# Optimization experiments

Hardware: AMD Instinct MI355X
Metric: run time of the kernel (lower is better)

## Reference

```python
import jax, jax.numpy as jnp
import numpy as np

TOP_K = 2

def moe_linear(x, router_w, experts_w):
    # x: [T, din]; router_w: [din, E]; experts_w: [E, din, dout]
    T = x.shape[0]
    E = experts_w.shape[0]
    probs = jax.nn.softmax(x @ router_w, axis=-1)            # [T, E]
    topv, topi = jax.lax.top_k(probs, TOP_K)                 # [T, k]
    topv = topv / jnp.sum(topv, axis=-1, keepdims=True)      # renormalize over selected experts
    w = jnp.zeros((T, E), x.dtype).at[jnp.arange(T)[:, None], topi].set(topv)  # dense routing weights
    y = jnp.zeros((T, experts_w.shape[2]), x.dtype)
    for e in range(E):  # small fixed expert loop; avoids [T,E,dout] intermediate
        y = y + w[:, e:e+1] * (x @ experts_w[e])
    return y

def setup_inputs() -> dict:
    key = jax.random.key(0)
    ks = jax.random.split(key, 7)
    B, S, H, I, E = 4, 2048, 1024, 3584, 8
    sH, sI = 1.0 / np.sqrt(H), 1.0 / np.sqrt(I)
    return {
        "hidden_state": jax.random.normal(ks[0], (B, S, H), jnp.float32),
        "gate_router": jax.random.normal(ks[1], (H, E), jnp.float32) * sH,
        "gate_experts": jax.random.normal(ks[2], (E, H, I), jnp.float32) * sH,
        "up_router": jax.random.normal(ks[3], (H, E), jnp.float32) * sH,
        "up_experts": jax.random.normal(ks[4], (E, H, I), jnp.float32) * sH,
        "down_router": jax.random.normal(ks[5], (I, E), jnp.float32) * sI,
        "down_experts": jax.random.normal(ks[6], (E, I, H), jnp.float32) * sI,
    }

def reference(hidden_state, gate_router, gate_experts, up_router, up_experts, down_router, down_experts):
    B, S, H = hidden_state.shape
    x = hidden_state.reshape(B * S, H)
    g = moe_linear(x, gate_router, gate_experts)             # [T, I]
    u = moe_linear(x, up_router, up_experts)                 # [T, I]
    h = jax.nn.silu(g) * u                                   # SwiGLU
    y = moe_linear(h, down_router, down_experts)             # [T, H]
    return y.reshape(B, S, H)
```

## Files before the change

kernel.cpp:

```cpp
#include <hip/hip_runtime.h>
#include <stdint.h>
#include <stdio.h>

#define T_TOK 8192
#define HDIM  1024
#define IDIM  3584
#define NEXP  8
#define NPAIR (T_TOK*2)
#define BK 32

typedef float          f32x4 __attribute__((ext_vector_type(4)));
typedef short          s16x8 __attribute__((ext_vector_type(8)));
typedef unsigned short u16x4 __attribute__((ext_vector_type(4)));
typedef unsigned short u16x8 __attribute__((ext_vector_type(8)));

__device__ __forceinline__ unsigned short f2bf_rne(float f) {
  unsigned u = __float_as_uint(f);
  u += 0x7FFFu + ((u >> 16) & 1u);
  return (unsigned short)(u >> 16);
}
__device__ __forceinline__ float bf2f(unsigned short h) {
  return __uint_as_float(((unsigned)h) << 16);
}

__device__ __forceinline__ void gld16(const void* gsrc, void* ldst) {
  typedef const unsigned int __attribute__((address_space(1))) GU;
  typedef unsigned int       __attribute__((address_space(3))) LU;
  __builtin_amdgcn_global_load_lds((GU*)(unsigned long long)gsrc,
                                   (LU*)(unsigned int)(unsigned long long)ldst,
                                   16, 0, 0);
}

__device__ __forceinline__ void top2_write(const float* acc, int t,
                                           int* __restrict__ topi,
                                           float* __restrict__ topw) {
  int i0 = 0; float l0 = acc[0];
#pragma unroll
  for (int e = 1; e < NEXP; e++) if (acc[e] > l0) { l0 = acc[e]; i0 = e; }
  int i1 = -1; float l1 = -3.4e38f;
#pragma unroll
  for (int e = 0; e < NEXP; e++) if (e != i0 && acc[e] > l1) { l1 = acc[e]; i1 = e; }
  float w0 = 1.f/(1.f + expf(l1 - l0));
  float w1 = 1.f/(1.f + expf(l0 - l1));
  topi[2*t]   = i0; topi[2*t+1] = i1;
  topw[2*t]   = w0; topw[2*t+1] = w1;
}

__global__ __launch_bounds__(256) void split_router(
    const float* __restrict__ X,
    const float* __restrict__ RWg, const float* __restrict__ RWu,
    unsigned short* __restrict__ xhi, unsigned short* __restrict__ xlo,
    int* __restrict__ tig, float* __restrict__ twg,
    int* __restrict__ tiu, float* __restrict__ twu) {
  int lane = threadIdx.x & 63;
  int t = blockIdx.x*4 + (threadIdx.x>>6);
  const f32x4* xr = (const f32x4*)(X + (long)t*HDIM);
  u16x4* hr = (u16x4*)(xhi + (long)t*HDIM);
  u16x4* lr = (u16x4*)(xlo + (long)t*HDIM);
  float ag[NEXP], au[NEXP];
#pragma unroll
  for (int e = 0; e < NEXP; e++) { ag[e] = 0.f; au[e] = 0.f; }
#pragma unroll
  for (int it = 0; it < HDIM/4/64; it++) {
    int c4 = it*64 + lane;
    f32x4 xv = xr[c4];
    u16x4 hh, ll;
#pragma unroll
    for (int j = 0; j < 4; j++) {
      unsigned short hb = f2bf_rne(xv[j]);
      hh[j] = hb;
      ll[j] = f2bf_rne(xv[j] - bf2f(hb));
    }
    hr[c4] = hh; lr[c4] = ll;
#pragma unroll
    for (int j = 0; j < 4; j++) {
      const float* wg = RWg + (long)(c4*4+j)*NEXP;
      const float* wu = RWu + (long)(c4*4+j)*NEXP;
#pragma unroll
      for (int e = 0; e < NEXP; e++) { ag[e] += xv[j]*wg[e]; au[e] += xv[j]*wu[e]; }
    }
  }
#pragma unroll
  for (int e = 0; e < NEXP; e++) {
    float vg = ag[e], vu = au[e];
#pragma unroll
    for (int o = 1; o < 64; o <<= 1) { vg += __shfl_xor(vg, o); vu += __shfl_xor(vu, o); }
    ag[e] = vg; au[e] = vu;
  }
  if (lane == 0) { top2_write(ag, t, tig, twg); top2_write(au, t, tiu, twu); }
}

__global__ void transpose_split3(const float* __restrict__ gex,
                                 unsigned short* __restrict__ wg_hi,
                                 unsigned short* __restrict__ wg_lo,
                                 const float* __restrict__ uex,
                                 unsigned short* __restrict__ wu_hi,
                                 unsigned short* __restrict__ wu_lo,
                                 const float* __restrict__ dex,
                                 unsigned short* __restrict__ wd_hi) {
  __shared__ float t[32][33];
  int z = blockIdx.z;
  const float* W; unsigned short *hi, *lo; int K, N, k0, n0;
  if (z < NEXP)        { W = gex; hi = wg_hi; lo = wg_lo; K = HDIM; N = IDIM;
                         n0 = blockIdx.x*32; k0 = blockIdx.y*32; }
  else if (z < 2*NEXP) { W = uex; hi = wu_hi; lo = wu_lo; K = HDIM; N = IDIM;
                         n0 = blockIdx.x*32; k0 = blockIdx.y*32; }
  else                 { W = dex; hi = wd_hi; lo = nullptr; K = IDIM; N = HDIM;
                         k0 = blockIdx.x*32; n0 = blockIdx.y*32; }
  long base = (long)(z & 7) * K * N;
  int id = threadIdx.y*8 + threadIdx.x;
  int lrr = id >> 3, lcq = id & 7;
  f32x4 v = *(const f32x4*)&W[base + (long)(k0+lrr)*N + n0 + lcq*4];
  t[lrr][lcq*4+0] = v[0]; t[lrr][lcq*4+1] = v[1];
  t[lrr][lcq*4+2] = v[2]; t[lrr][lcq*4+3] = v[3];
  __syncthreads();
  int n = threadIdx.y, kq = threadIdx.x;
  u16x4 h, l;
#pragma unroll
  for (int r = 0; r < 4; r++) {
    float f = t[kq*4+r][n];
    unsigned short hb = f2bf_rne(f);
    h[r] = hb;
    l[r] = f2bf_rne(f - bf2f(hb));
  }
  long o = base + (long)(n0+n)*K + k0 + kq*4;
  *(u16x4*)&hi[o] = h;
  if (lo) *(u16x4*)&lo[o] = l;
}

__device__ __forceinline__ void perm_body(const int* __restrict__ topi,
                                          const float* __restrict__ topw,
                                          int* __restrict__ offs,
                                          int* __restrict__ ptok,
                                          float* __restrict__ pw, int e) {
  int tid = threadIdx.x, lane = tid & 63, wv = tid >> 6;
  __shared__ int cnt[NEXP];
  __shared__ int wsum[4];
  if (tid < NEXP) cnt[tid] = 0;
  __syncthreads();
  for (int p = tid; p < NPAIR; p += 256) atomicAdd(&cnt[topi[p]], 1);
  __syncthreads();
  int base = 0;
#pragma unroll
  for (int e2 = 0; e2 < NEXP; e2++) if (e2 < e) base += cnt[e2];
  if (tid == 0) { offs[e] = base; if (e == NEXP-1) offs[NEXP] = base + cnt[e]; }
  for (int p0 = 0; p0 < NPAIR; p0 += 256) {
    int p = p0 + tid;
    bool m = (topi[p] == e);
    unsigned long long b = __ballot(m);
    int lp = __popcll(b & ((1ull << lane) - 1ull));
    if (lane == 0) wsum[wv] = __popcll(b);
    __syncthreads();
    int woff = 0;
#pragma unroll
    for (int w2 = 0; w2 < 4; w2++) if (w2 < wv) woff += wsum[w2];
    int tot = wsum[0] + wsum[1] + wsum[2] + wsum[3];
    if (m) { int dst = base + woff + lp; ptok[dst] = p >> 1; pw[dst] = topw[p]; }
    base += tot;
    __syncthreads();
  }
}
__global__ __launch_bounds__(256) void build_perm(const int* topi, const float* topw,
                                                  int* offs, int* ptok, float* pw) {
  perm_body(topi, topw, offs, ptok, pw, blockIdx.x);
}
__global__ __launch_bounds__(256) void build_perm2(
    const int* tig, const float* twg, int* offsg, int* ptokg, float* pwg,
    const int* tiu, const float* twu, int* offsu, int* ptoku, float* pwu) {
  if (blockIdx.x < NEXP) perm_body(tig, twg, offsg, ptokg, pwg, blockIdx.x);
  else                   perm_body(tiu, twu, offsu, ptoku, pwu, blockIdx.x - NEXP);
}

__global__ __launch_bounds__(512) void moe_gemm3_mt(
    const unsigned short* __restrict__ Ahi, const unsigned short* __restrict__ Alo,
    const unsigned short* __restrict__ Bhi, const unsigned short* __restrict__ Blo,
    const int* __restrict__ offs, const int* __restrict__ ptok,
    const float* __restrict__ pw, float* __restrict__ out)
{
  const int e = blockIdx.z;
  const int beg = offs[e];
  const int cnt = offs[e+1] - beg;
  const int m0 = blockIdx.y * 256;
  if (m0 >= cnt) return;
  const int n0 = blockIdx.x * 256;

  __shared__ unsigned short As[2][2][256*32];
  __shared__ unsigned short Bs[2][2][256*32];
  __shared__ int   stok[256];
  __shared__ float swt[256];

  const int tid = threadIdx.x, lane = tid & 63, wv = tid >> 6;
  if (tid < 256) {
    int i = m0 + tid;
    stok[tid] = ptok[beg + (i < cnt ? i : 0)];
    swt[tid]  = (i < cnt) ? pw[beg + i] : 0.f;
  }
  __syncthreads();

  const int srow = lane >> 2;
  const int lc   = ((lane & 3) - ((lane >> 3) & 3)) & 3;
  const long aoff0 = (long)stok[wv*32 +      srow]*HDIM + lc*8;
  const long aoff1 = (long)stok[wv*32 + 16 + srow]*HDIM + lc*8;
  const long boff0 = ((long)e*IDIM + n0 + wv*32 +      srow)*HDIM + lc*8;
  const long boff1 = ((long)e*IDIM + n0 + wv*32 + 16 + srow)*HDIM + lc*8;
  const int dst0 = (wv*32     )*32;
  const int dst1 = (wv*32 + 16)*32;

#define STAGE_A(buf, kk) do {                                   \
    int kl_ = (kk)*32;                                          \
    gld16(Ahi + aoff0 + kl_, &As[buf][0][dst0]);                \
    gld16(Ahi + aoff1 + kl_, &As[buf][0][dst1]);                \
    gld16(Alo + aoff0 + kl_, &As[buf][1][dst0]);                \
    gld16(Alo + aoff1 + kl_, &As[buf][1][dst1]);                \
  } while (0)
#define STAGE_B(buf, kk) do {                                   \
    int kl_ = (kk)*32;                                          \
    gld16(Bhi + boff0 + kl_, &Bs[buf][0][dst0]);                \
    gld16(Bhi + boff1 + kl_, &Bs[buf][0][dst1]);                \
    gld16(Blo + boff0 + kl_, &Bs[buf][1][dst0]);                \
    gld16(Blo + boff1 + kl_, &Bs[buf][1][dst1]);                \
  } while (0)

  const int fl = lane & 15, fg = lane >> 4;
  const int pks = (((fg + (fl >> 1)) & 3) << 3);
  const int wm = wv >> 2, wn = wv & 3;
  const int arow = wm * 128;
  const int bcol = wn * 64;

  f32x4 acc[8][4];
#pragma unroll
  for (int m = 0; m < 8; m++)
#pragma unroll
    for (int n = 0; n < 4; n++) acc[m][n] = {0.f, 0.f, 0.f, 0.f};

  STAGE_A(0, 0);
  STAGE_B(0, 0);
  __syncthreads();

  int cur = 0;
  for (int kt = 0; kt < HDIM/BK; ++kt) {
    const bool st = (kt + 1 < HDIM/BK);
    s16x8 ahf[8], bhi4[4], blo4[4];

    if (st) STAGE_A(cur^1, kt + 1);
#pragma unroll
    for (int n = 0; n < 4; n++)
      bhi4[n] = *(const s16x8*)&Bs[cur][0][(bcol + n*16 + fl)*32 + pks];
#pragma unroll
    for (int n = 0; n < 4; n++)
      blo4[n] = *(const s16x8*)&Bs[cur][1][(bcol + n*16 + fl)*32 + pks];
#pragma unroll
    for (int i = 0; i < 8; i++)
      ahf[i] = *(const s16x8*)&As[cur][0][(arow + i*16 + fl)*32 + pks];
    __builtin_amdgcn_s_setprio(1);
#pragma unroll
    for (int i = 0; i < 8; i++)
#pragma unroll
      for (int n = 0; n < 4; n++)
        acc[i][n] = __builtin_amdgcn_mfma_f32_16x16x32_bf16(ahf[i], bhi4[n], acc[i][n], 0,0,0);
    __builtin_amdgcn_s_setprio(0);

    if (st) STAGE_B(cur^1, kt + 1);
    __builtin_amdgcn_s_setprio(1);
#pragma unroll
    for (int i = 0; i < 8; i++)
#pragma unroll
      for (int n = 0; n < 4; n++)
        acc[i][n] = __builtin_amdgcn_mfma_f32_16x16x32_bf16(ahf[i], blo4[n], acc[i][n], 0,0,0);
    __builtin_amdgcn_s_setprio(0);

#pragma unroll
    for (int i = 0; i < 8; i++)
      ahf[i] = *(const s16x8*)&As[cur][1][(arow + i*16 + fl)*32 + pks];
    __builtin_amdgcn_s_setprio(1);
#pragma unroll
    for (int i = 0; i < 8; i++)
#pragma unroll
      for (int n = 0; n < 4; n++)
        acc[i][n] = __builtin_amdgcn_mfma_f32_16x16x32_bf16(ahf[i], bhi4[n], acc[i][n], 0,0,0);
    __builtin_amdgcn_s_setprio(0);

    __syncthreads();
    cur ^= 1;
  }
#undef STAGE_A
#undef STAGE_B

#pragma unroll
  for (int m = 0; m < 8; m++)
#pragma unroll
    for (int r = 0; r < 4; r++) {
      int lrow = arow + m*16 + fg*4 + r;
      if (m0 + lrow < cnt) {
        float wt = swt[lrow];
        long ob = (long)stok[lrow]*IDIM + n0 + bcol + fl;
#pragma unroll
        for (int n = 0; n < 4; n++)
          atomicAdd(&out[ob + n*16], wt * acc[m][n][r]);
      }
    }
}

__global__ __launch_bounds__(256) void swiglu_router_bf(
    const float* __restrict__ g, const float* __restrict__ u,
    unsigned short* __restrict__ hb,
    const float* __restrict__ RW,
    int* __restrict__ topi, float* __restrict__ topw) {
  int lane = threadIdx.x & 63;
  int t = blockIdx.x*4 + (threadIdx.x>>6);
  const f32x4* gr = (const f32x4*)(g + (long)t*IDIM);
  const f32x4* ur = (const f32x4*)(u + (long)t*IDIM);
  u16x4*       hr = (u16x4*)(hb + (long)t*IDIM);
  float acc[NEXP];
#pragma unroll
  for (int e = 0; e < NEXP; e++) acc[e] = 0.f;
#pragma unroll
  for (int it = 0; it < IDIM/4/64; it++) {
    int c4 = it*64 + lane;
    f32x4 gv = gr[c4], uv = ur[c4], hv;
    u16x4 hh;
#pragma unroll
    for (int j = 0; j < 4; j++) {
      float x = gv[j];
      hv[j] = x * uv[j] / (1.f + expf(-x));
      hh[j] = f2bf_rne(hv[j]);
    }
    hr[c4] = hh;
#pragma unroll
    for (int j = 0; j < 4; j++) {
      const float* wr = RW + (long)(c4*4+j)*NEXP;
#pragma unroll
      for (int e = 0; e < NEXP; e++) acc[e] += hv[j]*wr[e];
    }
  }
#pragma unroll
  for (int e = 0; e < NEXP; e++) {
    float v = acc[e];
#pragma unroll
    for (int o = 1; o < 64; o <<= 1) v += __shfl_xor(v, o);
    acc[e] = v;
  }
  if (lane == 0) top2_write(acc, t, topi, topw);
}

__global__ __launch_bounds__(256) void moe_gemm_down_bf(
    const unsigned short* __restrict__ Hb, const unsigned short* __restrict__ Bw,
    const int* __restrict__ offs, const int* __restrict__ ptok,
    const float* __restrict__ pw, float* __restrict__ out)
{
  const int K = IDIM, N = HDIM;
  const int e = blockIdx.z;
  const int beg = offs[e];
  const int cnt = offs[e+1] - beg;
  const int m0 = blockIdx.y * 128;
  if (m0 >= cnt) return;
  const int n0 = blockIdx.x * 128;

  __shared__ unsigned short As[2][128*32], Bs[2][128*32];
  __shared__ int   stok[128];
  __shared__ float swt[128];

  const int tid = threadIdx.x, lane = tid & 63, wv = tid >> 6;
  if (tid < 128) {
    int i = m0 + tid;
    stok[tid] = ptok[beg + (i < cnt ? i : 0)];
    swt[tid]  = (i < cnt) ? pw[beg + i] : 0.f;
  }
  __syncthreads();

  const int srow = lane >> 2;
  const int lc   = ((lane & 3) - ((lane >> 3) & 3)) & 3;
  const long aoff0 = (long)stok[wv*32 +      srow]*K + lc*8;
  const long aoff1 = (long)stok[wv*32 + 16 + srow]*K + lc*8;
  const long boff0 = ((long)e*N + n0 + wv*32 +      srow)*K + lc*8;
  const long boff1 = ((long)e*N + n0 + wv*32 + 16 + srow)*K + lc*8;
  const int dst0 = (wv*32     )*32;
  const int dst1 = (wv*32 + 16)*32;

#define STAGE(buf, kt) do {                                 \
    int kl_ = (kt)*32;                                      \
    gld16(Hb + aoff0 + kl_, &As[buf][dst0]);                \
    gld16(Hb + aoff1 + kl_, &As[buf][dst1]);                \
    gld16(Bw + boff0 + kl_, &Bs[buf][dst0]);                \
    gld16(Bw + boff1 + kl_, &Bs[buf][dst1]);                \
  } while (0)

  const int fl = lane & 15, fg = lane >> 4;
  const int pks = (((fg + (fl >> 1)) & 3) << 3);
  const int arow = (wv >> 1)*64, bcol = (wv & 1)*64;

  f32x4 acc[4][4];
#pragma unroll
  for (int m = 0; m < 4; m++)
#pragma unroll
    for (int n = 0; n < 4; n++) acc[m][n] = {0.f, 0.f, 0.f, 0.f};

  STAGE(0, 0);
  __syncthreads();

  int cur = 0;
  for (int kt = 0; kt < K/BK; ++kt) {
    if (kt + 1 < K/BK) STAGE(cur^1, kt + 1);

    s16x8 ahf[4], bhf[4];
#pragma unroll
    for (int i = 0; i < 4; i++) {
      ahf[i] = *(const s16x8*)&As[cur][(arow + i*16 + fl)*32 + pks];
      bhf[i] = *(const s16x8*)&Bs[cur][(bcol + i*16 + fl)*32 + pks];
    }
    __builtin_amdgcn_s_setprio(1);
#pragma unroll
    for (int i = 0; i < 4; i++)
#pragma unroll
      for (int n = 0; n < 4; n++)
        acc[i][n] = __builtin_amdgcn_mfma_f32_16x16x32_bf16(ahf[i], bhf[n], acc[i][n], 0,0,0);
    __builtin_amdgcn_s_setprio(0);

    __syncthreads();
    cur ^= 1;
  }
#undef STAGE

#pragma unroll
  for (int m = 0; m < 4; m++)
#pragma unroll
    for (int r = 0; r < 4; r++) {
      int lrow = arow + m*16 + fg*4 + r;
      if (m0 + lrow < cnt) {
        float wt = swt[lrow];
        long ob = (long)stok[lrow]*N + n0 + bcol + fl;
#pragma unroll
        for (int n = 0; n < 4; n++)
          atomicAdd(&out[ob + n*16], wt * acc[m][n][r]);
      }
    }
}

extern "C" void kernel_launch(void* const* d_in, const int* in_sizes, int n_in,
                              void* d_out, int out_size, void* d_ws, size_t ws_size,
                              hipStream_t stream)
{
  (void)in_sizes; (void)n_in;
  const float* x   = (const float*)d_in[0];
  const float* grt = (const float*)d_in[1];
  const float* gex = (const float*)d_in[2];
  const float* urt = (const float*)d_in[3];
  const float* uex = (const float*)d_in[4];
  const float* drt = (const float*)d_in[5];
  const float* dex = (const float*)d_in[6];
  float* out = (float*)d_out;

  char* base = (char*)d_ws;
  size_t off = 0;
  auto alloc = [&](size_t b) -> void* {
    void* r = base + off;
    off = (off + b + 255) & ~(size_t)255;
    return r;
  };
  const size_t szXH = (size_t)T_TOK*HDIM*2;
  const size_t szW  = (size_t)NEXP*HDIM*IDIM*2;
  const size_t szGI = (size_t)T_TOK*IDIM*4;

  unsigned short* xhi   = (unsigned short*)alloc(szXH);
  unsigned short* xlo   = (unsigned short*)alloc(szXH);
  unsigned short* wg_hi = (unsigned short*)alloc(szW);
  unsigned short* wg_lo = (unsigned short*)alloc(szW);
  unsigned short* wu_hi = (unsigned short*)alloc(szW);
  unsigned short* wu_lo = (unsigned short*)alloc(szW);
  unsigned short* wd_hi = (unsigned short*)alloc(szW);
  float* gbuf = (float*)alloc(szGI);
  int*   topi_g = (int*)alloc(NPAIR*4);  float* topw_g = (float*)alloc(NPAIR*4);
  int*   topi_u = (int*)alloc(NPAIR*4);  float* topw_u = (float*)alloc(NPAIR*4);
  int*   topi_d = (int*)alloc(NPAIR*4);  float* topw_d = (float*)alloc(NPAIR*4);
  int* offs_g = (int*)alloc(64);
  int* offs_u = (int*)alloc(64);
  int* offs_d = (int*)alloc(64);
  int*   ptok_g = (int*)alloc(NPAIR*4);  float* pw_g = (float*)alloc(NPAIR*4);
  int*   ptok_u = (int*)alloc(NPAIR*4);  float* pw_u = (float*)alloc(NPAIR*4);
  int*   ptok_d = (int*)alloc(NPAIR*4);  float* pw_d = (float*)alloc(NPAIR*4);

  float*          ubuf = (float*)wg_hi;
  unsigned short* hbuf = wu_lo;

  if (off > ws_size) {
    fprintf(stderr, "[moe] ws too small: need %zu bytes, have %zu\n", off, ws_size);
    hipMemsetAsync(d_out, 0, (size_t)out_size*sizeof(float), stream);
    return;
  }

  hipMemsetAsync(gbuf, 0, szGI, stream);
  hipMemsetAsync(d_out, 0, (size_t)out_size*sizeof(float), stream);

  transpose_split3<<<dim3(IDIM/32, HDIM/32, 3*NEXP), dim3(8,32), 0, stream>>>(
      gex, wg_hi, wg_lo, uex, wu_hi, wu_lo, dex, wd_hi);
  split_router<<<T_TOK/4, 256, 0, stream>>>(x, grt, urt, xhi, xlo,
                                            topi_g, topw_g, topi_u, topw_u);
  build_perm2<<<2*NEXP, 256, 0, stream>>>(topi_g, topw_g, offs_g, ptok_g, pw_g,
                                          topi_u, topw_u, offs_u, ptok_u, pw_u);

  moe_gemm3_mt<<<dim3(IDIM/256, 32, NEXP), 512, 0, stream>>>(
      xhi, xlo, wg_hi, wg_lo, offs_g, ptok_g, pw_g, gbuf);

  hipMemsetAsync(ubuf, 0, szGI, stream);
  moe_gemm3_mt<<<dim3(IDIM/256, 32, NEXP), 512, 0, stream>>>(
      xhi, xlo, wu_hi, wu_lo, offs_u, ptok_u, pw_u, ubuf);

  swiglu_router_bf<<<T_TOK/4, 256, 0, stream>>>(gbuf, ubuf, hbuf, drt, topi_d, topw_d);
  build_perm<<<NEXP, 256, 0, stream>>>(topi_d, topw_d, offs_d, ptok_d, pw_d);

  moe_gemm_down_bf<<<dim3(HDIM/128, 64, NEXP), 256, 0, stream>>>(
      hbuf, wd_hi, offs_d, ptok_d, pw_d, out);
}
```

Measured before the change: 1.537 ms.

## Replace double-buffered direct-to-LDS loads with register-staged single LDS buffer

The gate/up expert GEMM kernel drops its double-buffered LDS tiles, which were filled by direct global-to-LDS loads. It now prefetches the next K-tile into registers while computing on a single LDS buffer, then writes the registers to LDS after a barrier. This halves the LDS footprint, which could allow more resident blocks per CU. In exchange it adds an extra barrier per K-step, uses more VGPRs for staging, and loses the asynchronous global-to-LDS path.

New measurement: 1.606 ms. +4.5%, slower.

```diff
diff --git a/kernel.cpp b/kernel.cpp
--- a/kernel.cpp
+++ b/kernel.cpp
@@ -171,7 +171,7 @@
   else                   perm_body(tiu, twu, offsu, ptoku, pwu, blockIdx.x - NEXP);
 }
 
-__global__ __launch_bounds__(512) void moe_gemm3_mt(
+__global__ __launch_bounds__(512) void moe_gemm3_sb(
     const unsigned short* __restrict__ Ahi, const unsigned short* __restrict__ Alo,
     const unsigned short* __restrict__ Bhi, const unsigned short* __restrict__ Blo,
     const int* __restrict__ offs, const int* __restrict__ ptok,
@@ -184,8 +184,8 @@
   if (m0 >= cnt) return;
   const int n0 = blockIdx.x * 256;
 
-  __shared__ unsigned short As[2][2][256*32];
-  __shared__ unsigned short Bs[2][2][256*32];
+  __shared__ unsigned short As[2][256*32];
+  __shared__ unsigned short Bs[2][256*32];
   __shared__ int   stok[256];
   __shared__ float swt[256];
 
@@ -203,22 +203,26 @@
   const long aoff1 = (long)stok[wv*32 + 16 + srow]*HDIM + lc*8;
   const long boff0 = ((long)e*IDIM + n0 + wv*32 +      srow)*HDIM + lc*8;
   const long boff1 = ((long)e*IDIM + n0 + wv*32 + 16 + srow)*HDIM + lc*8;
-  const int dst0 = (wv*32     )*32;
-  const int dst1 = (wv*32 + 16)*32;
-
-#define STAGE_A(buf, kk) do {                                   \
-    int kl_ = (kk)*32;                                          \
-    gld16(Ahi + aoff0 + kl_, &As[buf][0][dst0]);                \
-    gld16(Ahi + aoff1 + kl_, &As[buf][0][dst1]);                \
-    gld16(Alo + aoff0 + kl_, &As[buf][1][dst0]);                \
-    gld16(Alo + aoff1 + kl_, &As[buf][1][dst1]);                \
+  const int wdst0 = (wv*32     )*32 + lane*8;
+  const int wdst1 = (wv*32 + 16)*32 + lane*8;
+
+  u16x8 ra0, ra1, ra2, ra3, rb0, rb1, rb2, rb3;
+
+#define LOADR(kk) do { int kl_ = (kk)*32;                        \
+    ra0 = *(const u16x8*)(Ahi + aoff0 + kl_);                    \
+    ra1 = *(const u16x8*)(Ahi + aoff1 + kl_);                    \
+    ra2 = *(const u16x8*)(Alo + aoff0 + kl_);                    \
+    ra3 = *(const u16x8*)(Alo + aoff1 + kl_);                    \
+    rb0 = *(const u16x8*)(Bhi + boff0 + kl_);                    \
+    rb1 = *(const u16x8*)(Bhi + boff1 + kl_);                    \
+    rb2 = *(const u16x8*)(Blo + boff0 + kl_);                    \
+    rb3 = *(const u16x8*)(Blo + boff1 + kl_);                    \
   } while (0)
-#define STAGE_B(buf, kk) do {                                   \
-    int kl_ = (kk)*32;                                          \
-    gld16(Bhi + boff0 + kl_, &Bs[buf][0][dst0]);                \
-    gld16(Bhi + boff1 + kl_, &Bs[buf][0][dst1]);                \
-    gld16(Blo + boff0 + kl_, &Bs[buf][1][dst0]);                \
-    gld16(Blo + boff1 + kl_, &Bs[buf][1][dst1]);                \
+#define WRITE_LDS() do {                                         \
+    *(u16x8*)&As[0][wdst0] = ra0;  *(u16x8*)&As[0][wdst1] = ra1; \
+    *(u16x8*)&As[1][wdst0] = ra2;  *(u16x8*)&As[1][wdst1] = ra3; \
+    *(u16x8*)&Bs[0][wdst0] = rb0;  *(u16x8*)&Bs[0][wdst1] = rb1; \
+    *(u16x8*)&Bs[1][wdst0] = rb2;  *(u16x8*)&Bs[1][wdst1] = rb3; \
   } while (0)
 
   const int fl = lane & 15, fg = lane >> 4;
@@ -233,25 +237,24 @@
 #pragma unroll
     for (int n = 0; n < 4; n++) acc[m][n] = {0.f, 0.f, 0.f, 0.f};
 
-  STAGE_A(0, 0);
-  STAGE_B(0, 0);
-  __syncthreads();
-
-  int cur = 0;
+  LOADR(0);
+  WRITE_LDS();
+  __syncthreads();
+
   for (int kt = 0; kt < HDIM/BK; ++kt) {
     const bool st = (kt + 1 < HDIM/BK);
+    if (st) LOADR(kt + 1);
+
     s16x8 ahf[8], bhi4[4], blo4[4];
-
-    if (st) STAGE_A(cur^1, kt + 1);
 #pragma unroll
     for (int n = 0; n < 4; n++)
-      bhi4[n] = *(const s16x8*)&Bs[cur][0][(bcol + n*16 + fl)*32 + pks];
+      bhi4[n] = *(const s16x8*)&Bs[0][(bcol + n*16 + fl)*32 + pks];
 #pragma unroll
     for (int n = 0; n < 4; n++)
-      blo4[n] = *(const s16x8*)&Bs[cur][1][(bcol + n*16 + fl)*32 + pks];
+      blo4[n] = *(const s16x8*)&Bs[1][(bcol + n*16 + fl)*32 + pks];
 #pragma unroll
     for (int i = 0; i < 8; i++)
-      ahf[i] = *(const s16x8*)&As[cur][0][(arow + i*16 + fl)*32 + pks];
+      ahf[i] = *(const s16x8*)&As[0][(arow + i*16 + fl)*32 + pks];
     __builtin_amdgcn_s_setprio(1);
 #pragma unroll
     for (int i = 0; i < 8; i++)
@@ -260,7 +263,6 @@
         acc[i][n] = __builtin_amdgcn_mfma_f32_16x16x32_bf16(ahf[i], bhi4[n], acc[i][n], 0,0,0);
     __builtin_amdgcn_s_setprio(0);
 
-    if (st) STAGE_B(cur^1, kt + 1);
     __builtin_amdgcn_s_setprio(1);
 #pragma unroll
     for (int i = 0; i < 8; i++)
@@ -271,7 +273,7 @@
 
 #pragma unroll
     for (int i = 0; i < 8; i++)
-      ahf[i] = *(const s16x8*)&As[cur][1][(arow + i*16 + fl)*32 + pks];
+      ahf[i] = *(const s16x8*)&As[1][(arow + i*16 + fl)*32 + pks];
     __builtin_amdgcn_s_setprio(1);
 #pragma unroll
     for (int i = 0; i < 8; i++)
@@ -281,10 +283,10 @@
     __builtin_amdgcn_s_setprio(0);
 
     __syncthreads();
-    cur ^= 1;
-  }
-#undef STAGE_A
-#undef STAGE_B
+    if (st) { WRITE_LDS(); __syncthreads(); }
+  }
+#undef LOADR
+#undef WRITE_LDS
 
 #pragma unroll
   for (int m = 0; m < 8; m++)
@@ -498,11 +500,11 @@
   build_perm2<<<2*NEXP, 256, 0, stream>>>(topi_g, topw_g, offs_g, ptok_g, pw_g,
                                           topi_u, topw_u, offs_u, ptok_u, pw_u);
 
-  moe_gemm3_mt<<<dim3(IDIM/256, 32, NEXP), 512, 0, stream>>>(
+  moe_gemm3_sb<<<dim3(IDIM/256, 32, NEXP), 512, 0, stream>>>(
       xhi, xlo, wg_hi, wg_lo, offs_g, ptok_g, pw_g, gbuf);
 
   hipMemsetAsync(ubuf, 0, szGI, stream);
-  moe_gemm3_mt<<<dim3(IDIM/256, 32, NEXP), 512, 0, stream>>>(
+  moe_gemm3_sb<<<dim3(IDIM/256, 32, NEXP), 512, 0, stream>>>(
       xhi, xlo, wu_hi, wu_lo, offs_u, ptok_u, pw_u, ubuf);
 
   swiglu_router_bf<<<T_TOK/4, 256, 0, stream>>>(gbuf, ubuf, hbuf, drt, topi_d, topw_d);
```

## Split 256x256 MoE GEMM tile across 16 waves instead of 8

Applied to the files above, without the earlier changes.

The gate/up grouped GEMM now launches 1024 threads (16 waves) per block on the same 256x256 output tile, so each wave covers a 64x64 sub-tile with half the accumulators and A fragments. Each wave issues half as many staging loads per k-step. This lowers per-wave register pressure and puts more waves on each CU to hide latency. The cost is more LDS fragment reads overall, since B fragments are re-read by more waves, plus heavier barrier synchronisation across 16 waves.

Measured after the change: 1.545 ms. No clear change (+0.5%).

```diff
diff --git a/kernel.cpp b/kernel.cpp
--- a/kernel.cpp
+++ b/kernel.cpp
@@ -171,7 +171,7 @@
   else                   perm_body(tiu, twu, offsu, ptoku, pwu, blockIdx.x - NEXP);
 }
 
-__global__ __launch_bounds__(512) void moe_gemm3_mt(
+__global__ __launch_bounds__(1024) void moe_gemm3_w16(
     const unsigned short* __restrict__ Ahi, const unsigned short* __restrict__ Alo,
     const unsigned short* __restrict__ Bhi, const unsigned short* __restrict__ Blo,
     const int* __restrict__ offs, const int* __restrict__ ptok,
@@ -199,37 +199,26 @@
 
   const int srow = lane >> 2;
   const int lc   = ((lane & 3) - ((lane >> 3) & 3)) & 3;
-  const long aoff0 = (long)stok[wv*32 +      srow]*HDIM + lc*8;
-  const long aoff1 = (long)stok[wv*32 + 16 + srow]*HDIM + lc*8;
-  const long boff0 = ((long)e*IDIM + n0 + wv*32 +      srow)*HDIM + lc*8;
-  const long boff1 = ((long)e*IDIM + n0 + wv*32 + 16 + srow)*HDIM + lc*8;
-  const int dst0 = (wv*32     )*32;
-  const int dst1 = (wv*32 + 16)*32;
-
-#define STAGE_A(buf, kk) do {                                   \
-    int kl_ = (kk)*32;                                          \
-    gld16(Ahi + aoff0 + kl_, &As[buf][0][dst0]);                \
-    gld16(Ahi + aoff1 + kl_, &As[buf][0][dst1]);                \
-    gld16(Alo + aoff0 + kl_, &As[buf][1][dst0]);                \
-    gld16(Alo + aoff1 + kl_, &As[buf][1][dst1]);                \
-  } while (0)
-#define STAGE_B(buf, kk) do {                                   \
-    int kl_ = (kk)*32;                                          \
-    gld16(Bhi + boff0 + kl_, &Bs[buf][0][dst0]);                \
-    gld16(Bhi + boff1 + kl_, &Bs[buf][0][dst1]);                \
-    gld16(Blo + boff0 + kl_, &Bs[buf][1][dst0]);                \
-    gld16(Blo + boff1 + kl_, &Bs[buf][1][dst1]);                \
-  } while (0)
+  const long aoff = (long)stok[wv*16 + srow]*HDIM + lc*8;
+  const long boff = ((long)e*IDIM + n0 + wv*16 + srow)*HDIM + lc*8;
+  const int dst = (wv*16)*32;
+
+#define STAGE_A(buf, kk) do { int kl_ = (kk)*32;                \
+    gld16(Ahi + aoff + kl_, &As[buf][0][dst]);                  \
+    gld16(Alo + aoff + kl_, &As[buf][1][dst]); } while (0)
+#define STAGE_B(buf, kk) do { int kl_ = (kk)*32;                \
+    gld16(Bhi + boff + kl_, &Bs[buf][0][dst]);                  \
+    gld16(Blo + boff + kl_, &Bs[buf][1][dst]); } while (0)
 
   const int fl = lane & 15, fg = lane >> 4;
   const int pks = (((fg + (fl >> 1)) & 3) << 3);
   const int wm = wv >> 2, wn = wv & 3;
-  const int arow = wm * 128;
+  const int arow = wm * 64;
   const int bcol = wn * 64;
 
-  f32x4 acc[8][4];
-#pragma unroll
-  for (int m = 0; m < 8; m++)
+  f32x4 acc[4][4];
+#pragma unroll
+  for (int m = 0; m < 4; m++)
 #pragma unroll
     for (int n = 0; n < 4; n++) acc[m][n] = {0.f, 0.f, 0.f, 0.f};
 
@@ -240,7 +229,7 @@
   int cur = 0;
   for (int kt = 0; kt < HDIM/BK; ++kt) {
     const bool st = (kt + 1 < HDIM/BK);
-    s16x8 ahf[8], bhi4[4], blo4[4];
+    s16x8 ahf[4], bhi4[4], blo4[4];
 
     if (st) STAGE_A(cur^1, kt + 1);
 #pragma unroll
@@ -250,11 +239,11 @@
     for (int n = 0; n < 4; n++)
       blo4[n] = *(const s16x8*)&Bs[cur][1][(bcol + n*16 + fl)*32 + pks];
 #pragma unroll
-    for (int i = 0; i < 8; i++)
+    for (int i = 0; i < 4; i++)
       ahf[i] = *(const s16x8*)&As[cur][0][(arow + i*16 + fl)*32 + pks];
     __builtin_amdgcn_s_setprio(1);
 #pragma unroll
-    for (int i = 0; i < 8; i++)
+    for (int i = 0; i < 4; i++)
 #pragma unroll
       for (int n = 0; n < 4; n++)
         acc[i][n] = __builtin_amdgcn_mfma_f32_16x16x32_bf16(ahf[i], bhi4[n], acc[i][n], 0,0,0);
@@ -263,18 +252,18 @@
     if (st) STAGE_B(cur^1, kt + 1);
     __builtin_amdgcn_s_setprio(1);
 #pragma unroll
-    for (int i = 0; i < 8; i++)
+    for (int i = 0; i < 4; i++)
 #pragma unroll
       for (int n = 0; n < 4; n++)
         acc[i][n] = __builtin_amdgcn_mfma_f32_16x16x32_bf16(ahf[i], blo4[n], acc[i][n], 0,0,0);
     __builtin_amdgcn_s_setprio(0);
 
 #pragma unroll
-    for (int i = 0; i < 8; i++)
+    for (int i = 0; i < 4; i++)
       ahf[i] = *(const s16x8*)&As[cur][1][(arow + i*16 + fl)*32 + pks];
     __builtin_amdgcn_s_setprio(1);
 #pragma unroll
-    for (int i = 0; i < 8; i++)
+    for (int i = 0; i < 4; i++)
 #pragma unroll
       for (int n = 0; n < 4; n++)
         acc[i][n] = __builtin_amdgcn_mfma_f32_16x16x32_bf16(ahf[i], bhi4[n], acc[i][n], 0,0,0);
@@ -287,7 +276,7 @@
 #undef STAGE_B
 
 #pragma unroll
-  for (int m = 0; m < 8; m++)
+  for (int m = 0; m < 4; m++)
 #pragma unroll
     for (int r = 0; r < 4; r++) {
       int lrow = arow + m*16 + fg*4 + r;
@@ -498,11 +487,11 @@
   build_perm2<<<2*NEXP, 256, 0, stream>>>(topi_g, topw_g, offs_g, ptok_g, pw_g,
                                           topi_u, topw_u, offs_u, ptok_u, pw_u);
 
-  moe_gemm3_mt<<<dim3(IDIM/256, 32, NEXP), 512, 0, stream>>>(
+  moe_gemm3_w16<<<dim3(IDIM/256, 32, NEXP), 1024, 0, stream>>>(
       xhi, xlo, wg_hi, wg_lo, offs_g, ptok_g, pw_g, gbuf);
 
   hipMemsetAsync(ubuf, 0, szGI, stream);
-  moe_gemm3_mt<<<dim3(IDIM/256, 32, NEXP), 512, 0, stream>>>(
+  moe_gemm3_w16<<<dim3(IDIM/256, 32, NEXP), 1024, 0, stream>>>(
       xhi, xlo, wu_hi, wu_lo, offs_u, ptok_u, pw_u, ubuf);
 
   swiglu_router_bf<<<T_TOK/4, 256, 0, stream>>>(gbuf, ubuf, hbuf, drt, topi_d, topw_d);
```
